# Optimization experiments

Measured on AMD Instinct MI355X. Metric: run time of the kernel, lower is better.

Reference implementation:

```python
import jax, jax.numpy as jnp
import numpy as np

N_NODES = 50000
N_EDGES = 800000
IN_CH, HID_CH, OUT_CH = 128, 256, 128


def _glorot(key, shape):
    fan_in, fan_out = shape[1], shape[0]
    lim = float(np.sqrt(6.0 / (fan_in + fan_out)))
    return jax.random.uniform(key, shape, jnp.float32, -lim, lim)


def setup_inputs() -> dict:
    key = jax.random.key(0)
    ks = jax.random.split(key, 8)
    x = jax.random.normal(ks[0], (N_NODES, IN_CH), jnp.float32)
    edge_index = jax.random.randint(ks[1], (2, N_EDGES), 0, N_NODES, jnp.int64)
    return {
        "x": x,
        "edge_index": edge_index,
        # layer 1: SAGEConv(128 -> 256): lin_l (with bias) on aggregated, lin_r (no bias) on root
        "W1l": _glorot(ks[2], (HID_CH, IN_CH)),
        "b1l": jnp.zeros((HID_CH,), jnp.float32),
        "W1r": _glorot(ks[3], (HID_CH, IN_CH)),
        # layer 2: SAGEConv(256 -> 128)
        "W2l": _glorot(ks[4], (OUT_CH, HID_CH)),
        "b2l": jnp.zeros((OUT_CH,), jnp.float32),
        "W2r": _glorot(ks[5], (OUT_CH, HID_CH)),
    }


def _sage_conv(x, src, dst, Wl, bl, Wr, n_nodes):
    # mean-aggregate neighbor (source) features at destination nodes
    msg = x[src]                                                   # [E, C] gather
    agg = jax.ops.segment_sum(msg, dst, num_segments=n_nodes)      # [N, C]
    deg = jax.ops.segment_sum(jnp.ones((src.shape[0],), x.dtype), dst,
                              num_segments=n_nodes)                # [N]
    mean = agg / jnp.maximum(deg, 1.0)[:, None]                    # zero-degree -> 0
    return mean @ Wl.T + bl + x @ Wr.T


def reference(x, edge_index, W1l, b1l, W1r, W2l, b2l, W2r):
    src, dst = edge_index[0], edge_index[1]
    n = x.shape[0]
    h = _sage_conv(x, src, dst, W1l, b1l, W1r, n)
    h = jax.nn.relu(h)  # dropout is identity in eval mode
    out = _sage_conv(h, src, dst, W2l, b2l, W2r, n)
    return out
```

## Files before the change

### kernel.cpp

```cpp
#include <hip/hip_runtime.h>

#define N_NODES 50000
#define IN_CH   128
#define HID_CH  256
#define OUT_CH  128

#define NB    196
#define NWG   64
#define NBNW  (NB * NWG)
#define SCHUNK 49

#define XBLK  3125
#define WBLK  64

#define LSTR 72

typedef __attribute__((ext_vector_type(8))) short bf16x8;
typedef __attribute__((ext_vector_type(4))) float f32x4;

__device__ __forceinline__ unsigned short f32_bf16_rne(float f) {
    unsigned u = __float_as_uint(f);
    unsigned r = u + 0x7fff + ((u >> 16) & 1);
    return (unsigned short)(r >> 16);
}
__device__ __forceinline__ float bf16lo_f32(unsigned u) { return __uint_as_float(u << 16); }
__device__ __forceinline__ float bf16hi_f32(unsigned u) { return __uint_as_float(u & 0xffff0000u); }

__device__ __forceinline__ void cvt8(const float* __restrict__ in,
                                     unsigned short* __restrict__ outp, size_t j)
{
    const float4* p = reinterpret_cast<const float4*>(in) + 2 * j;
    float4 a = p[0], b = p[1];
    alignas(16) unsigned short t[8] = {
        f32_bf16_rne(a.x), f32_bf16_rne(a.y), f32_bf16_rne(a.z), f32_bf16_rne(a.w),
        f32_bf16_rne(b.x), f32_bf16_rne(b.y), f32_bf16_rne(b.z), f32_bf16_rne(b.w)};
    *reinterpret_cast<int4*>(outp + 8 * j) = *reinterpret_cast<const int4*>(t);
}

__global__ __launch_bounds__(256) void prep_kernel(
    const int* __restrict__ src, const int* __restrict__ dst,
    int* __restrict__ counts, int E, int chunk,
    const float* __restrict__ x, unsigned short* __restrict__ xb,
    const float* __restrict__ W1l, const float* __restrict__ W1r,
    const float* __restrict__ W2l, const float* __restrict__ W2r,
    unsigned short* __restrict__ W1lb, unsigned short* __restrict__ W1rb,
    unsigned short* __restrict__ W2lb, unsigned short* __restrict__ W2rb)
{
    const int b = blockIdx.x;
    if (b < NWG) {
        __shared__ int h[NB];
        for (int i = threadIdx.x; i < NB; i += 256) h[i] = 0;
        __syncthreads();
        const int e0 = b * chunk;
        const int e1 = min(e0 + chunk, E);
        for (int e = e0 + threadIdx.x; e < e1; e += 256) {
            int s = src[e], d = dst[e];
            if ((unsigned)s < (unsigned)N_NODES && (unsigned)d < (unsigned)N_NODES)
                atomicAdd(&h[d >> 8], 1);
        }
        __syncthreads();
        for (int i = threadIdx.x; i < NB; i += 256)
            counts[i * NWG + b] = h[i];
    } else if (b < NWG + XBLK) {
        size_t j = (size_t)(b - NWG) * 256 + threadIdx.x;
        cvt8(x, xb, j);
    } else {
        int idx = (b - NWG - XBLK) * 256 + threadIdx.x;
        int seg = idx >> 12, j = idx & 4095;
        const float* in = (seg == 0) ? W1l : (seg == 1) ? W1r : (seg == 2) ? W2l : W2r;
        unsigned short* o = (seg == 0) ? W1lb : (seg == 1) ? W1rb : (seg == 2) ? W2lb : W2rb;
        cvt8(in, o, (size_t)j);
    }
}

__global__ __launch_bounds__(256) void scan_all_kernel(
    const int* __restrict__ counts, int* __restrict__ S)
{
    __shared__ int tot[256];
    const int t = threadIdx.x;
    const int base = t * SCHUNK;
    int loc[SCHUNK];
    int sum = 0;
#pragma unroll
    for (int k = 0; k < SCHUNK; ++k) {
        loc[k] = sum;
        sum += counts[base + k];
    }
    tot[t] = sum;
    __syncthreads();
    for (int off = 1; off < 256; off <<= 1) {
        int v = (t >= off) ? tot[t - off] : 0;
        __syncthreads();
        if (t >= off) tot[t] += v;
        __syncthreads();
    }
    int offv = (t == 0) ? 0 : tot[t - 1];
#pragma unroll
    for (int k = 0; k < SCHUNK; ++k)
        S[base + k] = loc[k] + offv;
    if (t == 255) S[NBNW] = offv + sum;
}

__global__ __launch_bounds__(256) void bscatter_kernel(
    const int* __restrict__ src, const int* __restrict__ dst,
    const int* __restrict__ S, int* __restrict__ pairs, int E, int chunk)
{
    __shared__ int cur[NB];
    const int w = blockIdx.x;
    for (int i = threadIdx.x; i < NB; i += 256) cur[i] = S[i * NWG + w];
    __syncthreads();
    const int e0 = w * chunk;
    const int e1 = min(e0 + chunk, E);
    for (int e = e0 + threadIdx.x; e < e1; e += 256) {
        int s = src[e], d = dst[e];
        if ((unsigned)s < (unsigned)N_NODES && (unsigned)d < (unsigned)N_NODES) {
            int pos = atomicAdd(&cur[d >> 8], 1);
            pairs[pos] = (s << 8) | (d & 255);
        }
    }
}

__global__ __launch_bounds__(256) void bsort_kernel(
    const int* __restrict__ pairs, const int* __restrict__ S,
    int* __restrict__ rowptr, int* __restrict__ colidx)
{
    __shared__ int hcnt[256];
    __shared__ int hcur[256];
    const int b = blockIdx.x;
    const int start = S[b * NWG];
    const int endv  = (b == NB - 1) ? S[NBNW] : S[(b + 1) * NWG];

    hcnt[threadIdx.x] = 0;
    __syncthreads();
    for (int e = start + threadIdx.x; e < endv; e += 256)
        atomicAdd(&hcnt[pairs[e] & 255], 1);
    __syncthreads();
    for (int off = 1; off < 256; off <<= 1) {
        int t = (threadIdx.x >= off) ? hcnt[threadIdx.x - off] : 0;
        __syncthreads();
        if (threadIdx.x >= off) hcnt[threadIdx.x] += t;
        __syncthreads();
    }
    int offv = (threadIdx.x == 0) ? 0 : hcnt[threadIdx.x - 1];
    hcur[threadIdx.x] = offv;
    int node = (b << 8) + threadIdx.x;
    if (node < N_NODES) rowptr[node] = start + offv;
    if (b == NB - 1 && threadIdx.x == 0) rowptr[N_NODES] = endv;
    __syncthreads();
    for (int e = start + threadIdx.x; e < endv; e += 256) {
        int p = pairs[e];
        int pos = atomicAdd(&hcur[p & 255], 1);
        colidx[start + pos] = (unsigned)p >> 8;
    }
}

#define AGG_BODY(CH)                                                            \
    const int node = blockIdx.x * 4 + (threadIdx.x >> 6);                       \
    if (node >= N_NODES) return;                                                \
    const int lane = threadIdx.x & 63;                                          \
    const int grp = lane >> 4, ch = lane & 15;                                  \
    const int beg = rowptr[node], end = rowptr[node + 1];                       \
    float acc[8] = {};                                                          \
    int i = beg + grp;                                                          \
    for (; i + 4 < end; i += 8) {                                               \
        int s0 = colidx[i], s1 = colidx[i + 4];                                 \
        int4 v0 = *reinterpret_cast<const int4*>(feat + (size_t)s0 * CH + ch * 8); \
        int4 v1 = *reinterpret_cast<const int4*>(feat + (size_t)s1 * CH + ch * 8); \
        acc[0] += bf16lo_f32(v0.x); acc[1] += bf16hi_f32(v0.x);                 \
        acc[2] += bf16lo_f32(v0.y); acc[3] += bf16hi_f32(v0.y);                 \
        acc[4] += bf16lo_f32(v0.z); acc[5] += bf16hi_f32(v0.z);                 \
        acc[6] += bf16lo_f32(v0.w); acc[7] += bf16hi_f32(v0.w);                 \
        acc[0] += bf16lo_f32(v1.x); acc[1] += bf16hi_f32(v1.x);                 \
        acc[2] += bf16lo_f32(v1.y); acc[3] += bf16hi_f32(v1.y);                 \
        acc[4] += bf16lo_f32(v1.z); acc[5] += bf16hi_f32(v1.z);                 \
        acc[6] += bf16lo_f32(v1.w); acc[7] += bf16hi_f32(v1.w);                 \
    }                                                                           \
    if (i < end) {                                                              \
        int s0 = colidx[i];                                                     \
        int4 v0 = *reinterpret_cast<const int4*>(feat + (size_t)s0 * CH + ch * 8); \
        acc[0] += bf16lo_f32(v0.x); acc[1] += bf16hi_f32(v0.x);                 \
        acc[2] += bf16lo_f32(v0.y); acc[3] += bf16hi_f32(v0.y);                 \
        acc[4] += bf16lo_f32(v0.z); acc[5] += bf16hi_f32(v0.z);                 \
        acc[6] += bf16lo_f32(v0.w); acc[7] += bf16hi_f32(v0.w);                 \
    }                                                                           \
    _Pragma("unroll")                                                           \
    for (int j = 0; j < 8; ++j) {                                               \
        acc[j] += __shfl_xor(acc[j], 16);                                       \
        acc[j] += __shfl_xor(acc[j], 32);                                       \
    }                                                                           \
    const float sc = 1.0f / fmaxf((float)(end - beg), 1.0f);

__global__ __launch_bounds__(256) void agg1_kernel(
    const unsigned short* __restrict__ feat, const int* __restrict__ rowptr,
    const int* __restrict__ colidx, unsigned short* __restrict__ outp)
{
    AGG_BODY(IN_CH)
    if (grp == 0) {
        alignas(16) unsigned short t[8];
#pragma unroll
        for (int j = 0; j < 8; ++j) t[j] = f32_bf16_rne(acc[j] * sc);
        *reinterpret_cast<int4*>(outp + (size_t)node * IN_CH + ch * 8) =
            *reinterpret_cast<const int4*>(t);
    }
}

__global__ __launch_bounds__(256) void agg2_kernel(
    const unsigned short* __restrict__ feat, const int* __restrict__ rowptr,
    const int* __restrict__ colidx, float* __restrict__ out)
{
    AGG_BODY(OUT_CH)
    if (grp == 0) {
        float* o = out + (size_t)node * OUT_CH + ch * 8;
        float4 o0 = reinterpret_cast<float4*>(o)[0];
        float4 o1 = reinterpret_cast<float4*>(o)[1];
        o0.x += acc[0] * sc; o0.y += acc[1] * sc; o0.z += acc[2] * sc; o0.w += acc[3] * sc;
        o1.x += acc[4] * sc; o1.y += acc[5] * sc; o1.z += acc[6] * sc; o1.w += acc[7] * sc;
        reinterpret_cast<float4*>(o)[0] = o0;
        reinterpret_cast<float4*>(o)[1] = o1;
    }
}

__device__ __forceinline__ void stage64(
    const unsigned short* __restrict__ g, int ldg, int rowBase, int maxRow,
    int kBase, unsigned short* __restrict__ s, int tid)
{
#pragma unroll
    for (int it = 0; it < 4; ++it) {
        int c = tid + it * 256;
        int r = c >> 3;
        int off = (c & 7) * 8;
        int row = rowBase + r;
        if (row >= maxRow) row = maxRow - 1;
        int4 v = *reinterpret_cast<const int4*>(g + (size_t)row * ldg + kBase + off);
        *reinterpret_cast<int4*>(s + r * LSTR + off) = v;
    }
}

__device__ __forceinline__ void mfma_tile(
    const unsigned short* __restrict__ As, const unsigned short* __restrict__ Bs,
    int wm, int wn, int l16, int quad, f32x4 acc[4][4])
{
#pragma unroll
    for (int k0 = 0; k0 < 64; k0 += 32) {
        bf16x8 a[4], b[4];
#pragma unroll
        for (int i = 0; i < 4; ++i)
            a[i] = *reinterpret_cast<const bf16x8*>(
                As + (wm * 64 + i * 16 + l16) * LSTR + k0 + quad * 8);
#pragma unroll
        for (int j = 0; j < 4; ++j)
            b[j] = *reinterpret_cast<const bf16x8*>(
                Bs + (wn * 64 + j * 16 + l16) * LSTR + k0 + quad * 8);
#pragma unroll
        for (int i = 0; i < 4; ++i)
#pragma unroll
            for (int j = 0; j < 4; ++j)
                acc[i][j] = __builtin_amdgcn_mfma_f32_16x16x32_bf16(
                    a[i], b[j], acc[i][j], 0, 0, 0);
    }
}

__global__ __launch_bounds__(256) void gemm1_mfma(
    const unsigned short* __restrict__ mean1b, const unsigned short* __restrict__ xb,
    const unsigned short* __restrict__ W1lb,   const unsigned short* __restrict__ W1rb,
    const float* __restrict__ b1l, unsigned short* __restrict__ hb)
{
    __shared__ unsigned short As[128 * LSTR];
    __shared__ unsigned short Bs[128 * LSTR];
    const int tid = threadIdx.x;
    const int wid = tid >> 6, lane = tid & 63;
    const int wm = wid & 1, wn = wid >> 1;
    const int l16 = lane & 15, quad = lane >> 4;
    const int rowBase = blockIdx.x * 128;
    const int colBase = blockIdx.y * 128;

    f32x4 z = {0.f, 0.f, 0.f, 0.f};
    f32x4 acc[4][4];
#pragma unroll
    for (int i = 0; i < 4; ++i)
#pragma unroll
        for (int j = 0; j < 4; ++j) acc[i][j] = z;

#pragma unroll
    for (int op = 0; op < 2; ++op) {
        const unsigned short* A = op ? xb : mean1b;
        const unsigned short* B = op ? W1rb : W1lb;
#pragma unroll
        for (int kb = 0; kb < IN_CH; kb += 64) {
            __syncthreads();
            stage64(A, IN_CH, rowBase, N_NODES, kb, As, tid);
            stage64(B, IN_CH, colBase, HID_CH, kb, Bs, tid);
            __syncthreads();
            mfma_tile(As, Bs, wm, wn, l16, quad, acc);
        }
    }

#pragma unroll
    for (int j = 0; j < 4; ++j) {
        int col = colBase + wn * 64 + j * 16 + l16;
        float bv = b1l[col];
#pragma unroll
        for (int i = 0; i < 4; ++i) {
            int mBase = rowBase + wm * 64 + i * 16 + quad * 4;
#pragma unroll
            for (int r = 0; r < 4; ++r) {
                int m = mBase + r;
                if (m < N_NODES) {
                    float v = fmaxf(acc[i][j][r] + bv, 0.0f);
                    hb[(size_t)m * HID_CH + col] = f32_bf16_rne(v);
                }
            }
        }
    }
}

__global__ __launch_bounds__(256) void gemm2_mfma(
    const unsigned short* __restrict__ hb, const unsigned short* __restrict__ W2lb,
    const unsigned short* __restrict__ W2rb, const float* __restrict__ b2l,
    unsigned short* __restrict__ pb, float* __restrict__ out)
{
    __shared__ unsigned short As[128 * LSTR];
    __shared__ unsigned short Bs[128 * LSTR];
    const int tid = threadIdx.x;
    const int wid = tid >> 6, lane = tid & 63;
    const int wm = wid & 1, wn = wid >> 1;
    const int l16 = lane & 15, quad = lane >> 4;
    const int rowBase = blockIdx.x * 128;
    const unsigned short* B = blockIdx.y ? W2rb : W2lb;

    f32x4 z = {0.f, 0.f, 0.f, 0.f};
    f32x4 acc[4][4];
#pragma unroll
    for (int i = 0; i < 4; ++i)
#pragma unroll
        for (int j = 0; j < 4; ++j) acc[i][j] = z;

#pragma unroll
    for (int kb = 0; kb < HID_CH; kb += 64) {
        __syncthreads();
        stage64(hb, HID_CH, rowBase, N_NODES, kb, As, tid);
        stage64(B, HID_CH, 0, OUT_CH, kb, Bs, tid);
        __syncthreads();
        mfma_tile(As, Bs, wm, wn, l16, quad, acc);
    }

    if (blockIdx.y == 0) {
#pragma unroll
        for (int j = 0; j < 4; ++j) {
            int col = wn * 64 + j * 16 + l16;
#pragma unroll
            for (int i = 0; i < 4; ++i) {
                int mBase = rowBase + wm * 64 + i * 16 + quad * 4;
#pragma unroll
                for (int r = 0; r < 4; ++r) {
                    int m = mBase + r;
                    if (m < N_NODES)
                        pb[(size_t)m * OUT_CH + col] = f32_bf16_rne(acc[i][j][r]);
                }
            }
        }
    } else {
#pragma unroll
        for (int j = 0; j < 4; ++j) {
            int col = wn * 64 + j * 16 + l16;
            float bv = b2l[col];
#pragma unroll
            for (int i = 0; i < 4; ++i) {
                int mBase = rowBase + wm * 64 + i * 16 + quad * 4;
#pragma unroll
                for (int r = 0; r < 4; ++r) {
                    int m = mBase + r;
                    if (m < N_NODES)
                        out[(size_t)m * OUT_CH + col] = acc[i][j][r] + bv;
                }
            }
        }
    }
}

extern "C" void kernel_launch(void* const* d_in, const int* in_sizes, int n_in,
                              void* d_out, int out_size, void* d_ws, size_t ws_size,
                              hipStream_t stream)
{
    const float* x   = (const float*)d_in[0];
    const int*   ei  = (const int*)d_in[1];
    const float* W1l = (const float*)d_in[2];
    const float* b1l = (const float*)d_in[3];
    const float* W1r = (const float*)d_in[4];
    const float* W2l = (const float*)d_in[5];
    const float* b2l = (const float*)d_in[6];
    const float* W2r = (const float*)d_in[7];

    const int E = in_sizes[1] / 2;
    const int* src = ei;
    const int* dst = ei + E;

    char* ws = (char*)d_ws;
    size_t off = 0;
    auto alloc = [&](size_t bytes) {
        void* p = ws + off;
        off += (bytes + 255) & ~(size_t)255;
        return p;
    };
    unsigned short* xb     = (unsigned short*)alloc((size_t)N_NODES * IN_CH * 2);
    unsigned short* mean1b = (unsigned short*)alloc((size_t)N_NODES * IN_CH * 2);
    unsigned short* hb     = (unsigned short*)alloc((size_t)N_NODES * HID_CH * 2);
    unsigned short* pb     = (unsigned short*)alloc((size_t)N_NODES * OUT_CH * 2);
    unsigned short* W1lb   = (unsigned short*)alloc((size_t)HID_CH * IN_CH * 2);
    unsigned short* W1rb   = (unsigned short*)alloc((size_t)HID_CH * IN_CH * 2);
    unsigned short* W2lb   = (unsigned short*)alloc((size_t)OUT_CH * HID_CH * 2);
    unsigned short* W2rb   = (unsigned short*)alloc((size_t)OUT_CH * HID_CH * 2);
    int* counts = (int*)alloc((size_t)NBNW * 4);
    int* S      = (int*)alloc((size_t)(NBNW + 1) * 4);
    int* pairs  = (int*)alloc((size_t)E * 4);
    int* rowptr = (int*)alloc((size_t)(N_NODES + 1) * 4);
    int* colidx = (int*)alloc((size_t)E * 4);
    float* out = (float*)d_out;

    const int chunk = (E + NWG - 1) / NWG;

    prep_kernel<<<NWG + XBLK + WBLK, 256, 0, stream>>>(
        src, dst, counts, E, chunk, x, xb,
        W1l, W1r, W2l, W2r, W1lb, W1rb, W2lb, W2rb);
    scan_all_kernel<<<1, 256, 0, stream>>>(counts, S);
    bscatter_kernel<<<NWG, 256, 0, stream>>>(src, dst, S, pairs, E, chunk);
    bsort_kernel<<<NB, 256, 0, stream>>>(pairs, S, rowptr, colidx);

    const int aggBlocks = (N_NODES + 3) / 4;
    const int mBlocks = (N_NODES + 127) / 128;

    agg1_kernel<<<aggBlocks, 256, 0, stream>>>(xb, rowptr, colidx, mean1b);
    gemm1_mfma<<<dim3(mBlocks, HID_CH / 128), 256, 0, stream>>>(
        mean1b, xb, W1lb, W1rb, b1l, hb);
    gemm2_mfma<<<dim3(mBlocks, 2), 256, 0, stream>>>(hb, W2lb, W2rb, b2l, pb, out);
    agg2_kernel<<<aggBlocks, 256, 0, stream>>>(pb, rowptr, colidx, out);
}
```

Before: 261.1 us.

## Transpose MFMA output for vector epilogue stores and use contiguous per-group edge ranges

New measurement: 244.6 us. -6.3%, faster.

```diff
diff --git a/kernel.cpp b/kernel.cpp
--- a/kernel.cpp
+++ b/kernel.cpp
@@ -154,41 +154,43 @@
     }
 }
 
+#define ACCUM_ROW(v)                                            \
+    acc[0] += bf16lo_f32(v.x); acc[1] += bf16hi_f32(v.x);       \
+    acc[2] += bf16lo_f32(v.y); acc[3] += bf16hi_f32(v.y);       \
+    acc[4] += bf16lo_f32(v.z); acc[5] += bf16hi_f32(v.z);       \
+    acc[6] += bf16lo_f32(v.w); acc[7] += bf16hi_f32(v.w);
+
 #define AGG_BODY(CH)                                                            \
     const int node = blockIdx.x * 4 + (threadIdx.x >> 6);                       \
     if (node >= N_NODES) return;                                                \
     const int lane = threadIdx.x & 63;                                          \
     const int grp = lane >> 4, ch = lane & 15;                                  \
     const int beg = rowptr[node], end = rowptr[node + 1];                       \
+    const int len = end - beg;                                                  \
+    const int q = (len + 3) >> 2;                                               \
+    int j  = beg + grp * q;                                                     \
+    int j1 = min(j + q, end);                                                   \
     float acc[8] = {};                                                          \
-    int i = beg + grp;                                                          \
-    for (; i + 4 < end; i += 8) {                                               \
-        int s0 = colidx[i], s1 = colidx[i + 4];                                 \
+    for (; j + 3 < j1; j += 4) {                                                \
+        int s0 = colidx[j],     s1 = colidx[j + 1];                             \
+        int s2 = colidx[j + 2], s3 = colidx[j + 3];                             \
         int4 v0 = *reinterpret_cast<const int4*>(feat + (size_t)s0 * CH + ch * 8); \
         int4 v1 = *reinterpret_cast<const int4*>(feat + (size_t)s1 * CH + ch * 8); \
-        acc[0] += bf16lo_f32(v0.x); acc[1] += bf16hi_f32(v0.x);                 \
-        acc[2] += bf16lo_f32(v0.y); acc[3] += bf16hi_f32(v0.y);                 \
-        acc[4] += bf16lo_f32(v0.z); acc[5] += bf16hi_f32(v0.z);                 \
-        acc[6] += bf16lo_f32(v0.w); acc[7] += bf16hi_f32(v0.w);                 \
-        acc[0] += bf16lo_f32(v1.x); acc[1] += bf16hi_f32(v1.x);                 \
-        acc[2] += bf16lo_f32(v1.y); acc[3] += bf16hi_f32(v1.y);                 \
-        acc[4] += bf16lo_f32(v1.z); acc[5] += bf16hi_f32(v1.z);                 \
-        acc[6] += bf16lo_f32(v1.w); acc[7] += bf16hi_f32(v1.w);                 \
+        int4 v2 = *reinterpret_cast<const int4*>(feat + (size_t)s2 * CH + ch * 8); \
+        int4 v3 = *reinterpret_cast<const int4*>(feat + (size_t)s3 * CH + ch * 8); \
+        ACCUM_ROW(v0) ACCUM_ROW(v1) ACCUM_ROW(v2) ACCUM_ROW(v3)                 \
     }                                                                           \
-    if (i < end) {                                                              \
-        int s0 = colidx[i];                                                     \
+    for (; j < j1; ++j) {                                                       \
+        int s0 = colidx[j];                                                     \
         int4 v0 = *reinterpret_cast<const int4*>(feat + (size_t)s0 * CH + ch * 8); \
-        acc[0] += bf16lo_f32(v0.x); acc[1] += bf16hi_f32(v0.x);                 \
-        acc[2] += bf16lo_f32(v0.y); acc[3] += bf16hi_f32(v0.y);                 \
-        acc[4] += bf16lo_f32(v0.z); acc[5] += bf16hi_f32(v0.z);                 \
-        acc[6] += bf16lo_f32(v0.w); acc[7] += bf16hi_f32(v0.w);                 \
+        ACCUM_ROW(v0)                                                           \
     }                                                                           \
     _Pragma("unroll")                                                           \
-    for (int j = 0; j < 8; ++j) {                                               \
-        acc[j] += __shfl_xor(acc[j], 16);                                       \
-        acc[j] += __shfl_xor(acc[j], 32);                                       \
+    for (int k = 0; k < 8; ++k) {                                               \
+        acc[k] += __shfl_xor(acc[k], 16);                                       \
+        acc[k] += __shfl_xor(acc[k], 32);                                       \
     }                                                                           \
-    const float sc = 1.0f / fmaxf((float)(end - beg), 1.0f);
+    const float sc = 1.0f / fmaxf((float)len, 1.0f);
 
 __global__ __launch_bounds__(256) void agg1_kernel(
     const unsigned short* __restrict__ feat, const int* __restrict__ rowptr,
@@ -198,7 +200,7 @@
     if (grp == 0) {
         alignas(16) unsigned short t[8];
 #pragma unroll
-        for (int j = 0; j < 8; ++j) t[j] = f32_bf16_rne(acc[j] * sc);
+        for (int k = 0; k < 8; ++k) t[k] = f32_bf16_rne(acc[k] * sc);
         *reinterpret_cast<int4*>(outp + (size_t)node * IN_CH + ch * 8) =
             *reinterpret_cast<const int4*>(t);
     }
@@ -256,7 +258,7 @@
 #pragma unroll
             for (int j = 0; j < 4; ++j)
                 acc[i][j] = __builtin_amdgcn_mfma_f32_16x16x32_bf16(
-                    a[i], b[j], acc[i][j], 0, 0, 0);
+                    b[j], a[i], acc[i][j], 0, 0, 0);
     }
 }
 
@@ -296,20 +298,20 @@
     }
 
 #pragma unroll
-    for (int j = 0; j < 4; ++j) {
-        int col = colBase + wn * 64 + j * 16 + l16;
-        float bv = b1l[col];
-#pragma unroll
-        for (int i = 0; i < 4; ++i) {
-            int mBase = rowBase + wm * 64 + i * 16 + quad * 4;
-#pragma unroll
-            for (int r = 0; r < 4; ++r) {
-                int m = mBase + r;
-                if (m < N_NODES) {
-                    float v = fmaxf(acc[i][j][r] + bv, 0.0f);
-                    hb[(size_t)m * HID_CH + col] = f32_bf16_rne(v);
-                }
-            }
+    for (int i = 0; i < 4; ++i) {
+        int m = rowBase + wm * 64 + i * 16 + l16;
+        if (m >= N_NODES) continue;
+#pragma unroll
+        for (int j = 0; j < 4; ++j) {
+            int col = colBase + wn * 64 + j * 16 + quad * 4;
+            float4 bv = *reinterpret_cast<const float4*>(b1l + col);
+            alignas(8) unsigned short t[4];
+            t[0] = f32_bf16_rne(fmaxf(acc[i][j][0] + bv.x, 0.0f));
+            t[1] = f32_bf16_rne(fmaxf(acc[i][j][1] + bv.y, 0.0f));
+            t[2] = f32_bf16_rne(fmaxf(acc[i][j][2] + bv.z, 0.0f));
+            t[3] = f32_bf16_rne(fmaxf(acc[i][j][3] + bv.w, 0.0f));
+            *reinterpret_cast<uint2*>(hb + (size_t)m * HID_CH + col) =
+                *reinterpret_cast<const uint2*>(t);
         }
     }
 }
@@ -346,33 +348,36 @@
 
     if (blockIdx.y == 0) {
 #pragma unroll
-        for (int j = 0; j < 4; ++j) {
-            int col = wn * 64 + j * 16 + l16;
-#pragma unroll
-            for (int i = 0; i < 4; ++i) {
-                int mBase = rowBase + wm * 64 + i * 16 + quad * 4;
-#pragma unroll
-                for (int r = 0; r < 4; ++r) {
-                    int m = mBase + r;
-                    if (m < N_NODES)
-                        pb[(size_t)m * OUT_CH + col] = f32_bf16_rne(acc[i][j][r]);
-                }
+        for (int i = 0; i < 4; ++i) {
+            int m = rowBase + wm * 64 + i * 16 + l16;
+            if (m >= N_NODES) continue;
+#pragma unroll
+            for (int j = 0; j < 4; ++j) {
+                int col = wn * 64 + j * 16 + quad * 4;
+                alignas(8) unsigned short t[4];
+                t[0] = f32_bf16_rne(acc[i][j][0]);
+                t[1] = f32_bf16_rne(acc[i][j][1]);
+                t[2] = f32_bf16_rne(acc[i][j][2]);
+                t[3] = f32_bf16_rne(acc[i][j][3]);
+                *reinterpret_cast<uint2*>(pb + (size_t)m * OUT_CH + col) =
+                    *reinterpret_cast<const uint2*>(t);
             }
         }
     } else {
 #pragma unroll
-        for (int j = 0; j < 4; ++j) {
-            int col = wn * 64 + j * 16 + l16;
-            float bv = b2l[col];
-#pragma unroll
-            for (int i = 0; i < 4; ++i) {
-                int mBase = rowBase + wm * 64 + i * 16 + quad * 4;
-#pragma unroll
-                for (int r = 0; r < 4; ++r) {
-                    int m = mBase + r;
-                    if (m < N_NODES)
-                        out[(size_t)m * OUT_CH + col] = acc[i][j][r] + bv;
-                }
+        for (int i = 0; i < 4; ++i) {
+            int m = rowBase + wm * 64 + i * 16 + l16;
+            if (m >= N_NODES) continue;
+#pragma unroll
+            for (int j = 0; j < 4; ++j) {
+                int col = wn * 64 + j * 16 + quad * 4;
+                float4 bv = *reinterpret_cast<const float4*>(b2l + col);
+                float4 o;
+                o.x = acc[i][j][0] + bv.x;
+                o.y = acc[i][j][1] + bv.y;
+                o.z = acc[i][j][2] + bv.z;
+                o.w = acc[i][j][3] + bv.w;
+                *reinterpret_cast<float4*>(out + (size_t)m * OUT_CH + col) = o;
             }
         }
     }
```
